# Kernel optimization log

Measured on AMD Instinct MI355X. Metric: run time of the kernel, lower is better.

## Reference

```python
import jax, jax.numpy as jnp
import numpy as np

ATT_TIMES = 2
EPS = 1e-12  # torch F.normalize eps

N_NODES = 200000
EMB_DIM = 256
ATT_NUM = 2


def setup_inputs() -> dict:
    key = jax.random.key(0)
    k1, k2 = jax.random.split(key)
    x = jax.random.normal(k1, (N_NODES, EMB_DIM), dtype=jnp.float32)
    # glorot/xavier-normal init for the att_num projection matrices W_i
    std = float(np.sqrt(2.0 / (EMB_DIM + EMB_DIM)))
    W = jax.random.normal(k2, (ATT_NUM, EMB_DIM, EMB_DIM), dtype=jnp.float32) * std
    return {"x": x, "W": W}


def _one_attention(x, Wi):
    """One attention head (att_style='dot', att_weight=True), iterated ATT_TIMES."""
    xi = x
    out = None
    for _ in range(ATT_TIMES):
        temp = jnp.mean(xi, axis=0, keepdims=True)          # (1, D)
        h_avg = jnp.tanh(temp @ Wi)                          # (1, D)
        # 'dot' style: interact with W = identity -> scores = x @ h_avg^T, (N, 1)
        scores = xi @ h_avg.T                                # (N, 1)
        # F.normalize(p=1, dim=1) on an (N,1) column: divide by max(|v|, eps)
        norm = jnp.maximum(jnp.sum(jnp.abs(scores), axis=1, keepdims=True), EPS)
        att = jax.nn.sigmoid(scores / norm)                  # (N, 1)
        out = att.T @ xi                                     # (1, D)
        xi = xi * att                                        # re-weight for next round
    return out


def reference(x, W):
    att_num = W.shape[0]
    outs = [_one_attention(x, W[i]) for i in range(att_num)]
    return jnp.concatenate(outs, axis=1)                     # (1, att_num * D)
```

## Files before the change

### kernel.cpp

```cpp
#include <hip/hip_runtime.h>
#include <math.h>

#define NROWS 200000
#define D 256
#define F4_PER_ROW 64

#define NBLK 500
#define CHUNK 400
#define ITERS 25
#define RPB 8
#define RED_BLOCKS ((NBLK + RPB - 1) / RPB)

#define WS_C     0
#define WS_OUT1  256
#define WS_OUT2  768
#define WS_H1    1280
#define WS_H2    1792
#define WS_A     2304
#define WS_PART  402304
#define ZERO_CNT 1280

__device__ __forceinline__ float att_sigmoid(float s) {
    float t = s / fmaxf(fabsf(s), 1e-12f);
    return 1.0f / (1.0f + __expf(-t));
}

__device__ __forceinline__ float wave_sum(float v) {
#pragma unroll
    for (int off = 1; off < 64; off <<= 1) v += __shfl_xor(v, off);
    return v;
}

__global__ void zero_kernel(float* __restrict__ ws, float* __restrict__ out) {
    int i = blockIdx.x * blockDim.x + threadIdx.x;
    if (i < ZERO_CNT) ws[i] = 0.0f;
    if (i < 2 * D) out[i] = 0.0f;
}

__global__ void __launch_bounds__(256) colsum_kernel(const float* __restrict__ x,
                                                     float* __restrict__ part) {
    const int tid = threadIdx.x;
    const int lane = tid & 63;
    const int wv = tid >> 6;
    const int r0 = blockIdx.x * CHUNK + wv * 4;
    const float4* x4 = reinterpret_cast<const float4*>(x);
    float4 acc = make_float4(0.f, 0.f, 0.f, 0.f);
#pragma unroll 2
    for (int it = 0; it < ITERS; ++it) {
        size_t rb = (size_t)(r0 + it * 16) * F4_PER_ROW + lane;
        float4 v0 = x4[rb];
        float4 v1 = x4[rb + F4_PER_ROW];
        float4 v2 = x4[rb + 2 * F4_PER_ROW];
        float4 v3 = x4[rb + 3 * F4_PER_ROW];
        acc.x += (v0.x + v1.x) + (v2.x + v3.x);
        acc.y += (v0.y + v1.y) + (v2.y + v3.y);
        acc.z += (v0.z + v1.z) + (v2.z + v3.z);
        acc.w += (v0.w + v1.w) + (v2.w + v3.w);
    }
    __shared__ float4 sh[256];
    sh[tid] = acc;
    __syncthreads();
    if (tid < 64) {
        float4 a = sh[tid], b = sh[tid + 64], c = sh[tid + 128], d = sh[tid + 192];
        float4 s;
        s.x = (a.x + b.x) + (c.x + d.x);
        s.y = (a.y + b.y) + (c.y + d.y);
        s.z = (a.z + b.z) + (c.z + d.z);
        s.w = (a.w + b.w) + (c.w + d.w);
        reinterpret_cast<float4*>(part + blockIdx.x * 256)[tid] = s;
    }
}

__global__ void __launch_bounds__(256) reduce_parts(const float* __restrict__ src,
                                                    float* __restrict__ dst,
                                                    int nparts, int width) {
    const int tid = threadIdx.x;
    const int rlo = blockIdx.x * RPB;
    const int rhi = (rlo + RPB < nparts) ? (rlo + RPB) : nparts;
    for (int c = tid; c < width; c += 256) {
        float s0 = 0.f, s1 = 0.f;
        int r = rlo;
        for (; r + 1 < rhi; r += 2) {
            s0 += src[(size_t)r * width + c];
            s1 += src[(size_t)(r + 1) * width + c];
        }
        if (r < rhi) s0 += src[(size_t)r * width + c];
        atomicAdd(&dst[c], s0 + s1);
    }
}

__global__ void hproj_kernel(const float* __restrict__ W,
                             const float* __restrict__ vin, int vstride, float scale,
                             float* __restrict__ hout) {
    int head = blockIdx.x;
    int j = threadIdx.x;
    __shared__ float v[D];
    v[j] = vin[head * vstride + j] * scale;
    __syncthreads();
    const float* Wh = W + head * D * D;
    float acc = 0.0f;
#pragma unroll 8
    for (int k = 0; k < D; ++k) acc = fmaf(v[k], Wh[k * D + j], acc);
    hout[head * D + j] = tanhf(acc);
}

__global__ void __launch_bounds__(256) pass1_kernel(const float* __restrict__ x,
                                                    float* __restrict__ ws) {
    const float* h = ws + WS_H1;
    float* aA0 = ws + WS_A;
    float* aA1 = ws + WS_A + NROWS;
    float* part = ws + WS_PART;
    const int tid = threadIdx.x;
    const int lane = tid & 63;
    const int wv = tid >> 6;
    const int r0 = blockIdx.x * CHUNK + wv * 4;
    const float4* x4 = reinterpret_cast<const float4*>(x);
    float4 h0v = reinterpret_cast<const float4*>(h)[lane];
    float4 h1v = reinterpret_cast<const float4*>(h + D)[lane];
    float4 acc0 = make_float4(0.f, 0.f, 0.f, 0.f);
    float4 acc1 = make_float4(0.f, 0.f, 0.f, 0.f);
    for (int it = 0; it < ITERS; ++it) {
        const int rb = r0 + it * 16;
        float4 xv[4];
#pragma unroll
        for (int j = 0; j < 4; ++j) xv[j] = x4[(size_t)(rb + j) * F4_PER_ROW + lane];
        float d0[4], d1[4];
#pragma unroll
        for (int j = 0; j < 4; ++j) {
            d0[j] = fmaf(xv[j].x, h0v.x, fmaf(xv[j].y, h0v.y, fmaf(xv[j].z, h0v.z, xv[j].w * h0v.w)));
            d1[j] = fmaf(xv[j].x, h1v.x, fmaf(xv[j].y, h1v.y, fmaf(xv[j].z, h1v.z, xv[j].w * h1v.w)));
        }
#pragma unroll
        for (int j = 0; j < 4; ++j) { d0[j] = wave_sum(d0[j]); d1[j] = wave_sum(d1[j]); }
        float a0[4], a1[4];
#pragma unroll
        for (int j = 0; j < 4; ++j) {
            a0[j] = att_sigmoid(d0[j]);
            a1[j] = att_sigmoid(d1[j]);
            acc0.x = fmaf(a0[j], xv[j].x, acc0.x);
            acc0.y = fmaf(a0[j], xv[j].y, acc0.y);
            acc0.z = fmaf(a0[j], xv[j].z, acc0.z);
            acc0.w = fmaf(a0[j], xv[j].w, acc0.w);
            acc1.x = fmaf(a1[j], xv[j].x, acc1.x);
            acc1.y = fmaf(a1[j], xv[j].y, acc1.y);
            acc1.z = fmaf(a1[j], xv[j].z, acc1.z);
            acc1.w = fmaf(a1[j], xv[j].w, acc1.w);
        }
        if (lane == 0) {
            *reinterpret_cast<float4*>(aA0 + rb) = make_float4(a0[0], a0[1], a0[2], a0[3]);
        } else if (lane == 1) {
            *reinterpret_cast<float4*>(aA1 + rb) = make_float4(a1[0], a1[1], a1[2], a1[3]);
        }
    }
    __shared__ float4 sh[2][256];
    sh[0][tid] = acc0;
    sh[1][tid] = acc1;
    __syncthreads();
    if (tid < 128) {
        int hh = tid >> 6;
        int t = tid & 63;
        float4 a = sh[hh][t], b = sh[hh][t + 64], c = sh[hh][t + 128], d = sh[hh][t + 192];
        float4 s;
        s.x = (a.x + b.x) + (c.x + d.x);
        s.y = (a.y + b.y) + (c.y + d.y);
        s.z = (a.z + b.z) + (c.z + d.z);
        s.w = (a.w + b.w) + (c.w + d.w);
        reinterpret_cast<float4*>(part + blockIdx.x * 512)[tid] = s;
    }
}

__global__ void __launch_bounds__(256) pass2_kernel(const float* __restrict__ x,
                                                    float* __restrict__ ws) {
    const float* h = ws + WS_H2;
    const float* aA0 = ws + WS_A;
    const float* aA1 = ws + WS_A + NROWS;
    float* part = ws + WS_PART;
    const int tid = threadIdx.x;
    const int lane = tid & 63;
    const int wv = tid >> 6;
    const int r0 = blockIdx.x * CHUNK + wv * 4;
    const float4* x4 = reinterpret_cast<const float4*>(x);
    float4 h0v = reinterpret_cast<const float4*>(h)[lane];
    float4 h1v = reinterpret_cast<const float4*>(h + D)[lane];
    float4 acc0 = make_float4(0.f, 0.f, 0.f, 0.f);
    float4 acc1 = make_float4(0.f, 0.f, 0.f, 0.f);
    for (int it = 0; it < ITERS; ++it) {
        const int rb = r0 + it * 16;
        float4 xv[4];
#pragma unroll
        for (int j = 0; j < 4; ++j) xv[j] = x4[(size_t)(rb + j) * F4_PER_ROW + lane];
        float4 aa0 = *reinterpret_cast<const float4*>(aA0 + rb);
        float4 aa1 = *reinterpret_cast<const float4*>(aA1 + rb);
        float d0[4], d1[4];
#pragma unroll
        for (int j = 0; j < 4; ++j) {
            d0[j] = fmaf(xv[j].x, h0v.x, fmaf(xv[j].y, h0v.y, fmaf(xv[j].z, h0v.z, xv[j].w * h0v.w)));
            d1[j] = fmaf(xv[j].x, h1v.x, fmaf(xv[j].y, h1v.y, fmaf(xv[j].z, h1v.z, xv[j].w * h1v.w)));
        }
#pragma unroll
        for (int j = 0; j < 4; ++j) { d0[j] = wave_sum(d0[j]); d1[j] = wave_sum(d1[j]); }
        float w0[4], w1[4];
        w0[0] = att_sigmoid(aa0.x * d0[0]) * aa0.x;
        w0[1] = att_sigmoid(aa0.y * d0[1]) * aa0.y;
        w0[2] = att_sigmoid(aa0.z * d0[2]) * aa0.z;
        w0[3] = att_sigmoid(aa0.w * d0[3]) * aa0.w;
        w1[0] = att_sigmoid(aa1.x * d1[0]) * aa1.x;
        w1[1] = att_sigmoid(aa1.y * d1[1]) * aa1.y;
        w1[2] = att_sigmoid(aa1.z * d1[2]) * aa1.z;
        w1[3] = att_sigmoid(aa1.w * d1[3]) * aa1.w;
#pragma unroll
        for (int j = 0; j < 4; ++j) {
            acc0.x = fmaf(w0[j], xv[j].x, acc0.x);
            acc0.y = fmaf(w0[j], xv[j].y, acc0.y);
            acc0.z = fmaf(w0[j], xv[j].z, acc0.z);
            acc0.w = fmaf(w0[j], xv[j].w, acc0.w);
            acc1.x = fmaf(w1[j], xv[j].x, acc1.x);
            acc1.y = fmaf(w1[j], xv[j].y, acc1.y);
            acc1.z = fmaf(w1[j], xv[j].z, acc1.z);
            acc1.w = fmaf(w1[j], xv[j].w, acc1.w);
        }
    }
    __shared__ float4 sh[2][256];
    sh[0][tid] = acc0;
    sh[1][tid] = acc1;
    __syncthreads();
    if (tid < 128) {
        int hh = tid >> 6;
        int t = tid & 63;
        float4 a = sh[hh][t], b = sh[hh][t + 64], c = sh[hh][t + 128], d = sh[hh][t + 192];
        float4 s;
        s.x = (a.x + b.x) + (c.x + d.x);
        s.y = (a.y + b.y) + (c.y + d.y);
        s.z = (a.z + b.z) + (c.z + d.z);
        s.w = (a.w + b.w) + (c.w + d.w);
        reinterpret_cast<float4*>(part + blockIdx.x * 512)[tid] = s;
    }
}

extern "C" void kernel_launch(void* const* d_in, const int* in_sizes, int n_in,
                              void* d_out, int out_size, void* d_ws, size_t ws_size,
                              hipStream_t stream) {
    const float* x = (const float*)d_in[0];
    const float* W = (const float*)d_in[1];
    float* out = (float*)d_out;
    float* ws = (float*)d_ws;

    zero_kernel<<<dim3(5), dim3(256), 0, stream>>>(ws, out);
    colsum_kernel<<<dim3(NBLK), dim3(256), 0, stream>>>(x, ws + WS_PART);
    reduce_parts<<<dim3(RED_BLOCKS), dim3(256), 0, stream>>>(ws + WS_PART, ws + WS_C, NBLK, 256);
    hproj_kernel<<<dim3(2), dim3(256), 0, stream>>>(W, ws + WS_C, 0, 1.0f / NROWS, ws + WS_H1);
    pass1_kernel<<<dim3(NBLK), dim3(256), 0, stream>>>(x, ws);
    reduce_parts<<<dim3(RED_BLOCKS), dim3(256), 0, stream>>>(ws + WS_PART, ws + WS_OUT1, NBLK, 512);
    hproj_kernel<<<dim3(2), dim3(256), 0, stream>>>(W, ws + WS_OUT1, D, 1.0f / NROWS, ws + WS_H2);
    pass2_kernel<<<dim3(NBLK), dim3(256), 0, stream>>>(x, ws);
    reduce_parts<<<dim3(RED_BLOCKS), dim3(256), 0, stream>>>(ws + WS_PART, out, NBLK, 512);
}
```

Before: 186.1 us.

## Fuse partial reductions into projection kernels and software-pipeline row loads

Drops the zero kernel and the three atomic-based reduce_parts launches. The 500 per-block partials are now summed directly inside the head-projection kernel, and a dedicated two-block out_reduce writes the final output without atomics. This cuts the pipeline from nine launches to six. It also adds register double-buffering of the x rows (and the attention vectors in pass2) in colsum, pass1 and pass2 so the next loads are issued before the current compute. The fused reductions run on only two blocks each, which serialises the partial summation, and the prefetch raises register pressure.

```diff
diff --git a/kernel.cpp b/kernel.cpp
--- a/kernel.cpp
+++ b/kernel.cpp
@@ -3,22 +3,17 @@
 
 #define NROWS 200000
 #define D 256
-#define F4_PER_ROW 64
+#define F4 64
 
 #define NBLK 500
 #define CHUNK 400
 #define ITERS 25
-#define RPB 8
-#define RED_BLOCKS ((NBLK + RPB - 1) / RPB)
-
-#define WS_C     0
-#define WS_OUT1  256
-#define WS_OUT2  768
-#define WS_H1    1280
-#define WS_H2    1792
-#define WS_A     2304
-#define WS_PART  402304
-#define ZERO_CNT 1280
+
+#define WS_H1 0
+#define WS_H2 512
+#define WS_A  1024
+#define WS_P1 401024
+#define WS_P2 529024
 
 __device__ __forceinline__ float att_sigmoid(float s) {
     float t = s / fmaxf(fabsf(s), 1e-12f);
@@ -31,34 +26,38 @@
     return v;
 }
 
-__global__ void zero_kernel(float* __restrict__ ws, float* __restrict__ out) {
-    int i = blockIdx.x * blockDim.x + threadIdx.x;
-    if (i < ZERO_CNT) ws[i] = 0.0f;
-    if (i < 2 * D) out[i] = 0.0f;
+__device__ __forceinline__ float dot4(float4 a, float4 b) {
+    return fmaf(a.x, b.x, fmaf(a.y, b.y, fmaf(a.z, b.z, a.w * b.w)));
 }
 
 __global__ void __launch_bounds__(256) colsum_kernel(const float* __restrict__ x,
                                                      float* __restrict__ part) {
-    const int tid = threadIdx.x;
-    const int lane = tid & 63;
-    const int wv = tid >> 6;
-    const int r0 = blockIdx.x * CHUNK + wv * 4;
+    const int tid = threadIdx.x, lane = tid & 63, wv = tid >> 6;
     const float4* x4 = reinterpret_cast<const float4*>(x);
-    float4 acc = make_float4(0.f, 0.f, 0.f, 0.f);
-#pragma unroll 2
+    const size_t base = (size_t)(blockIdx.x * CHUNK + wv * 4) * F4 + lane;
+    float4 cur[4], nxt[4];
+#pragma unroll
+    for (int j = 0; j < 4; ++j) cur[j] = x4[base + j * F4];
+    float4 accA = make_float4(0.f, 0.f, 0.f, 0.f);
+    float4 accB = make_float4(0.f, 0.f, 0.f, 0.f);
     for (int it = 0; it < ITERS; ++it) {
-        size_t rb = (size_t)(r0 + it * 16) * F4_PER_ROW + lane;
-        float4 v0 = x4[rb];
-        float4 v1 = x4[rb + F4_PER_ROW];
-        float4 v2 = x4[rb + 2 * F4_PER_ROW];
-        float4 v3 = x4[rb + 3 * F4_PER_ROW];
-        acc.x += (v0.x + v1.x) + (v2.x + v3.x);
-        acc.y += (v0.y + v1.y) + (v2.y + v3.y);
-        acc.z += (v0.z + v1.z) + (v2.z + v3.z);
-        acc.w += (v0.w + v1.w) + (v2.w + v3.w);
-    }
+        if (it + 1 < ITERS) {
+            size_t nb = base + (size_t)(it + 1) * 16 * F4;
+#pragma unroll
+            for (int j = 0; j < 4; ++j) nxt[j] = x4[nb + j * F4];
+        }
+        accA.x += cur[0].x + cur[1].x; accB.x += cur[2].x + cur[3].x;
+        accA.y += cur[0].y + cur[1].y; accB.y += cur[2].y + cur[3].y;
+        accA.z += cur[0].z + cur[1].z; accB.z += cur[2].z + cur[3].z;
+        accA.w += cur[0].w + cur[1].w; accB.w += cur[2].w + cur[3].w;
+        if (it + 1 < ITERS) {
+#pragma unroll
+            for (int j = 0; j < 4; ++j) cur[j] = nxt[j];
+        }
+    }
+    accA.x += accB.x; accA.y += accB.y; accA.z += accB.z; accA.w += accB.w;
     __shared__ float4 sh[256];
-    sh[tid] = acc;
+    sh[tid] = accA;
     __syncthreads();
     if (tid < 64) {
         float4 a = sh[tid], b = sh[tid + 64], c = sh[tid + 128], d = sh[tid + 192];
@@ -71,37 +70,41 @@
     }
 }
 
-__global__ void __launch_bounds__(256) reduce_parts(const float* __restrict__ src,
-                                                    float* __restrict__ dst,
-                                                    int nparts, int width) {
-    const int tid = threadIdx.x;
-    const int rlo = blockIdx.x * RPB;
-    const int rhi = (rlo + RPB < nparts) ? (rlo + RPB) : nparts;
-    for (int c = tid; c < width; c += 256) {
-        float s0 = 0.f, s1 = 0.f;
-        int r = rlo;
-        for (; r + 1 < rhi; r += 2) {
-            s0 += src[(size_t)r * width + c];
-            s1 += src[(size_t)(r + 1) * width + c];
-        }
-        if (r < rhi) s0 += src[(size_t)r * width + c];
-        atomicAdd(&dst[c], s0 + s1);
-    }
-}
-
-__global__ void hproj_kernel(const float* __restrict__ W,
-                             const float* __restrict__ vin, int vstride, float scale,
-                             float* __restrict__ hout) {
-    int head = blockIdx.x;
-    int j = threadIdx.x;
-    __shared__ float v[D];
-    v[j] = vin[head * vstride + j] * scale;
+__global__ void __launch_bounds__(256) hproj_fused(const float* __restrict__ W,
+                                                   const float* __restrict__ part,
+                                                   int width, int headColMul, float scale,
+                                                   float* __restrict__ hout) {
+    const int head = blockIdx.x;
+    const int tid = threadIdx.x, lane = tid & 63, wv = tid >> 6;
+    const float* p = part + head * headColMul + lane * 4;
+    float4 s = make_float4(0.f, 0.f, 0.f, 0.f);
+    for (int i = 0; i < 25; ++i) {
+        float4 v[5];
+#pragma unroll
+        for (int k = 0; k < 5; ++k)
+            v[k] = *reinterpret_cast<const float4*>(p + (size_t)(wv + (i * 5 + k) * 4) * width);
+#pragma unroll
+        for (int k = 0; k < 5; ++k) {
+            s.x += v[k].x; s.y += v[k].y; s.z += v[k].z; s.w += v[k].w;
+        }
+    }
+    __shared__ float4 red[4][64];
+    __shared__ float vbuf[D];
+    red[wv][lane] = s;
+    __syncthreads();
+    if (tid < 64) {
+        float4 a = red[0][tid], b = red[1][tid], c = red[2][tid], d = red[3][tid];
+        vbuf[tid * 4 + 0] = ((a.x + b.x) + (c.x + d.x)) * scale;
+        vbuf[tid * 4 + 1] = ((a.y + b.y) + (c.y + d.y)) * scale;
+        vbuf[tid * 4 + 2] = ((a.z + b.z) + (c.z + d.z)) * scale;
+        vbuf[tid * 4 + 3] = ((a.w + b.w) + (c.w + d.w)) * scale;
+    }
     __syncthreads();
     const float* Wh = W + head * D * D;
     float acc = 0.0f;
 #pragma unroll 8
-    for (int k = 0; k < D; ++k) acc = fmaf(v[k], Wh[k * D + j], acc);
-    hout[head * D + j] = tanhf(acc);
+    for (int k = 0; k < D; ++k) acc = fmaf(vbuf[k], Wh[k * D + tid], acc);
+    hout[head * D + tid] = tanhf(acc);
 }
 
 __global__ void __launch_bounds__(256) pass1_kernel(const float* __restrict__ x,
@@ -109,27 +112,27 @@
     const float* h = ws + WS_H1;
     float* aA0 = ws + WS_A;
     float* aA1 = ws + WS_A + NROWS;
-    float* part = ws + WS_PART;
-    const int tid = threadIdx.x;
-    const int lane = tid & 63;
-    const int wv = tid >> 6;
+    float* part = ws + WS_P2;
+    const int tid = threadIdx.x, lane = tid & 63, wv = tid >> 6;
     const int r0 = blockIdx.x * CHUNK + wv * 4;
     const float4* x4 = reinterpret_cast<const float4*>(x);
-    float4 h0v = reinterpret_cast<const float4*>(h)[lane];
-    float4 h1v = reinterpret_cast<const float4*>(h + D)[lane];
+    const float4 h0v = reinterpret_cast<const float4*>(h)[lane];
+    const float4 h1v = reinterpret_cast<const float4*>(h + D)[lane];
     float4 acc0 = make_float4(0.f, 0.f, 0.f, 0.f);
     float4 acc1 = make_float4(0.f, 0.f, 0.f, 0.f);
+    const size_t base = (size_t)r0 * F4 + lane;
+    float4 cur[4], nxt[4];
+#pragma unroll
+    for (int j = 0; j < 4; ++j) cur[j] = x4[base + j * F4];
     for (int it = 0; it < ITERS; ++it) {
-        const int rb = r0 + it * 16;
-        float4 xv[4];
-#pragma unroll
-        for (int j = 0; j < 4; ++j) xv[j] = x4[(size_t)(rb + j) * F4_PER_ROW + lane];
+        if (it + 1 < ITERS) {
+            size_t nb = base + (size_t)(it + 1) * 16 * F4;
+#pragma unroll
+            for (int j = 0; j < 4; ++j) nxt[j] = x4[nb + j * F4];
+        }
         float d0[4], d1[4];
 #pragma unroll
-        for (int j = 0; j < 4; ++j) {
-            d0[j] = fmaf(xv[j].x, h0v.x, fmaf(xv[j].y, h0v.y, fmaf(xv[j].z, h0v.z, xv[j].w * h0v.w)));
-            d1[j] = fmaf(xv[j].x, h1v.x, fmaf(xv[j].y, h1v.y, fmaf(xv[j].z, h1v.z, xv[j].w * h1v.w)));
-        }
+        for (int j = 0; j < 4; ++j) { d0[j] = dot4(cur[j], h0v); d1[j] = dot4(cur[j], h1v); }
 #pragma unroll
         for (int j = 0; j < 4; ++j) { d0[j] = wave_sum(d0[j]); d1[j] = wave_sum(d1[j]); }
         float a0[4], a1[4];
@@ -137,19 +140,23 @@
         for (int j = 0; j < 4; ++j) {
             a0[j] = att_sigmoid(d0[j]);
             a1[j] = att_sigmoid(d1[j]);
-            acc0.x = fmaf(a0[j], xv[j].x, acc0.x);
-            acc0.y = fmaf(a0[j], xv[j].y, acc0.y);
-            acc0.z = fmaf(a0[j], xv[j].z, acc0.z);
-            acc0.w = fmaf(a0[j], xv[j].w, acc0.w);
-            acc1.x = fmaf(a1[j], xv[j].x, acc1.x);
-            acc1.y = fmaf(a1[j], xv[j].y, acc1.y);
-            acc1.z = fmaf(a1[j], xv[j].z, acc1.z);
-            acc1.w = fmaf(a1[j], xv[j].w, acc1.w);
-        }
-        if (lane == 0) {
+            acc0.x = fmaf(a0[j], cur[j].x, acc0.x);
+            acc0.y = fmaf(a0[j], cur[j].y, acc0.y);
+            acc0.z = fmaf(a0[j], cur[j].z, acc0.z);
+            acc0.w = fmaf(a0[j], cur[j].w, acc0.w);
+            acc1.x = fmaf(a1[j], cur[j].x, acc1.x);
+            acc1.y = fmaf(a1[j], cur[j].y, acc1.y);
+            acc1.z = fmaf(a1[j], cur[j].z, acc1.z);
+            acc1.w = fmaf(a1[j], cur[j].w, acc1.w);
+        }
+        const int rb = r0 + it * 16;
+        if (lane == 0)
             *reinterpret_cast<float4*>(aA0 + rb) = make_float4(a0[0], a0[1], a0[2], a0[3]);
-        } else if (lane == 1) {
+        else if (lane == 1)
             *reinterpret_cast<float4*>(aA1 + rb) = make_float4(a1[0], a1[1], a1[2], a1[3]);
+        if (it + 1 < ITERS) {
+#pragma unroll
+            for (int j = 0; j < 4; ++j) cur[j] = nxt[j];
         }
     }
     __shared__ float4 sh[2][256];
@@ -174,50 +181,58 @@
     const float* h = ws + WS_H2;
     const float* aA0 = ws + WS_A;
     const float* aA1 = ws + WS_A + NROWS;
-    float* part = ws + WS_PART;
-    const int tid = threadIdx.x;
-    const int lane = tid & 63;
-    const int wv = tid >> 6;
+    float* part = ws + WS_P2;
+    const int tid = threadIdx.x, lane = tid & 63, wv = tid >> 6;
     const int r0 = blockIdx.x * CHUNK + wv * 4;
     const float4* x4 = reinterpret_cast<const float4*>(x);
-    float4 h0v = reinterpret_cast<const float4*>(h)[lane];
-    float4 h1v = reinterpret_cast<const float4*>(h + D)[lane];
+    const float4 h0v = reinterpret_cast<const float4*>(h)[lane];
+    const float4 h1v = reinterpret_cast<const float4*>(h + D)[lane];
     float4 acc0 = make_float4(0.f, 0.f, 0.f, 0.f);
     float4 acc1 = make_float4(0.f, 0.f, 0.f, 0.f);
+    const size_t base = (size_t)r0 * F4 + lane;
+    float4 cur[4], nxt[4];
+    float4 caa0, caa1, naa0, naa1;
+#pragma unroll
+    for (int j = 0; j < 4; ++j) cur[j] = x4[base + j * F4];
+    caa0 = *reinterpret_cast<const float4*>(aA0 + r0);
+    caa1 = *reinterpret_cast<const float4*>(aA1 + r0);
     for (int it = 0; it < ITERS; ++it) {
-        const int rb = r0 + it * 16;
-        float4 xv[4];
-#pragma unroll
-        for (int j = 0; j < 4; ++j) xv[j] = x4[(size_t)(rb + j) * F4_PER_ROW + lane];
-        float4 aa0 = *reinterpret_cast<const float4*>(aA0 + rb);
-        float4 aa1 = *reinterpret_cast<const float4*>(aA1 + rb);
+        if (it + 1 < ITERS) {
+            size_t nb = base + (size_t)(it + 1) * 16 * F4;
+#pragma unroll
+            for (int j = 0; j < 4; ++j) nxt[j] = x4[nb + j * F4];
+            naa0 = *reinterpret_cast<const float4*>(aA0 + r0 + (it + 1) * 16);
+            naa1 = *reinterpret_cast<const float4*>(aA1 + r0 + (it + 1) * 16);
+        }
         float d0[4], d1[4];
 #pragma unroll
-        for (int j = 0; j < 4; ++j) {
-            d0[j] = fmaf(xv[j].x, h0v.x, fmaf(xv[j].y, h0v.y, fmaf(xv[j].z, h0v.z, xv[j].w * h0v.w)));
-            d1[j] = fmaf(xv[j].x, h1v.x, fmaf(xv[j].y, h1v.y, fmaf(xv[j].z, h1v.z, xv[j].w * h1v.w)));
-        }
+        for (int j = 0; j < 4; ++j) { d0[j] = dot4(cur[j], h0v); d1[j] = dot4(cur[j], h1v); }
 #pragma unroll
         for (int j = 0; j < 4; ++j) { d0[j] = wave_sum(d0[j]); d1[j] = wave_sum(d1[j]); }
         float w0[4], w1[4];
-        w0[0] = att_sigmoid(aa0.x * d0[0]) * aa0.x;
-        w0[1] = att_sigmoid(aa0.y * d0[1]) * aa0.y;
-        w0[2] = att_sigmoid(aa0.z * d0[2]) * aa0.z;
-        w0[3] = att_sigmoid(aa0.w * d0[3]) * aa0.w;
-        w1[0] = att_sigmoid(aa1.x * d1[0]) * aa1.x;
-        w1[1] = att_sigmoid(aa1.y * d1[1]) * aa1.y;
-        w1[2] = att_sigmoid(aa1.z * d1[2]) * aa1.z;
-        w1[3] = att_sigmoid(aa1.w * d1[3]) * aa1.w;
+        w0[0] = att_sigmoid(caa0.x * d0[0]) * caa0.x;
+        w0[1] = att_sigmoid(caa0.y * d0[1]) * caa0.y;
+        w0[2] = att_sigmoid(caa0.z * d0[2]) * caa0.z;
+        w0[3] = att_sigmoid(caa0.w * d0[3]) * caa0.w;
+        w1[0] = att_sigmoid(caa1.x * d1[0]) * caa1.x;
+        w1[1] = att_sigmoid(caa1.y * d1[1]) * caa1.y;
+        w1[2] = att_sigmoid(caa1.z * d1[2]) * caa1.z;
+        w1[3] = att_sigmoid(caa1.w * d1[3]) * caa1.w;
 #pragma unroll
         for (int j = 0; j < 4; ++j) {
-            acc0.x = fmaf(w0[j], xv[j].x, acc0.x);
-            acc0.y = fmaf(w0[j], xv[j].y, acc0.y);
-            acc0.z = fmaf(w0[j], xv[j].z, acc0.z);
-            acc0.w = fmaf(w0[j], xv[j].w, acc0.w);
-            acc1.x = fmaf(w1[j], xv[j].x, acc1.x);
-            acc1.y = fmaf(w1[j], xv[j].y, acc1.y);
-            acc1.z = fmaf(w1[j], xv[j].z, acc1.z);
-            acc1.w = fmaf(w1[j], xv[j].w, acc1.w);
+            acc0.x = fmaf(w0[j], cur[j].x, acc0.x);
+            acc0.y = fmaf(w0[j], cur[j].y, acc0.y);
+            acc0.z = fmaf(w0[j], cur[j].z, acc0.z);
+            acc0.w = fmaf(w0[j], cur[j].w, acc0.w);
+            acc1.x = fmaf(w1[j], cur[j].x, acc1.x);
+            acc1.y = fmaf(w1[j], cur[j].y, acc1.y);
+            acc1.z = fmaf(w1[j], cur[j].z, acc1.z);
+            acc1.w = fmaf(w1[j], cur[j].w, acc1.w);
+        }
+        if (it + 1 < ITERS) {
+#pragma unroll
+            for (int j = 0; j < 4; ++j) cur[j] = nxt[j];
+            caa0 = naa0; caa1 = naa1;
         }
     }
     __shared__ float4 sh[2][256];
@@ -237,6 +252,36 @@
     }
 }
 
+__global__ void __launch_bounds__(256) out_reduce(const float* __restrict__ part,
+                                                  float* __restrict__ out) {
+    const int head = blockIdx.x;
+    const int tid = threadIdx.x, lane = tid & 63, wv = tid >> 6;
+    const float* p = part + head * 256 + lane * 4;
+    float4 s = make_float4(0.f, 0.f, 0.f, 0.f);
+    for (int i = 0; i < 25; ++i) {
+        float4 v[5];
+#pragma unroll
+        for (int k = 0; k < 5; ++k)
+            v[k] = *reinterpret_cast<const float4*>(p + (size_t)(wv + (i * 5 + k) * 4) * 512);
+#pragma unroll
+        for (int k = 0; k < 5; ++k) {
+            s.x += v[k].x; s.y += v[k].y; s.z += v[k].z; s.w += v[k].w;
+        }
+    }
+    __shared__ float4 red[4][64];
+    red[wv][lane] = s;
+    __syncthreads();
+    if (tid < 64) {
+        float4 a = red[0][tid], b = red[1][tid], c = red[2][tid], d = red[3][tid];
+        float4 o;
+        o.x = (a.x + b.x) + (c.x + d.x);
+        o.y = (a.y + b.y) + (c.y + d.y);
+        o.z = (a.z + b.z) + (c.z + d.z);
+        o.w = (a.w + b.w) + (c.w + d.w);
+        reinterpret_cast<float4*>(out + head * 256)[tid] = o;
+    }
+}
+
 extern "C" void kernel_launch(void* const* d_in, const int* in_sizes, int n_in,
                               void* d_out, int out_size, void* d_ws, size_t ws_size,
                               hipStream_t stream) {
@@ -245,13 +290,10 @@
     float* out = (float*)d_out;
     float* ws = (float*)d_ws;
 
-    zero_kernel<<<dim3(5), dim3(256), 0, stream>>>(ws, out);
-    colsum_kernel<<<dim3(NBLK), dim3(256), 0, stream>>>(x, ws + WS_PART);
-    reduce_parts<<<dim3(RED_BLOCKS), dim3(256), 0, stream>>>(ws + WS_PART, ws + WS_C, NBLK, 256);
-    hproj_kernel<<<dim3(2), dim3(256), 0, stream>>>(W, ws + WS_C, 0, 1.0f / NROWS, ws + WS_H1);
+    colsum_kernel<<<dim3(NBLK), dim3(256), 0, stream>>>(x, ws + WS_P1);
+    hproj_fused<<<dim3(2), dim3(256), 0, stream>>>(W, ws + WS_P1, 256, 0, 1.0f / NROWS, ws + WS_H1);
     pass1_kernel<<<dim3(NBLK), dim3(256), 0, stream>>>(x, ws);
-    reduce_parts<<<dim3(RED_BLOCKS), dim3(256), 0, stream>>>(ws + WS_PART, ws + WS_OUT1, NBLK, 512);
-    hproj_kernel<<<dim3(2), dim3(256), 0, stream>>>(W, ws + WS_OUT1, D, 1.0f / NROWS, ws + WS_H2);
+    hproj_fused<<<dim3(2), dim3(256), 0, stream>>>(W, ws + WS_P2, 512, 256, 1.0f / NROWS, ws + WS_H2);
     pass2_kernel<<<dim3(NBLK), dim3(256), 0, stream>>>(x, ws);
-    reduce_parts<<<dim3(RED_BLOCKS), dim3(256), 0, stream>>>(ws + WS_PART, out, NBLK, 512);
-}
+    out_reduce<<<dim3(2), dim3(256), 0, stream>>>(ws + WS_P2, out);
+}
```

Measured after the change: 167.2 us. 10.1% less time.
